# Optimization experiments

Hardware: AMD Instinct MI355X
Metric: run time of the kernel (lower is better)

## Reference

```python
import jax, jax.numpy as jnp
import numpy as np

B, N, CIN, H, OUT, L, K = 8, 512, 64, 64, 64, 256, 3
EPS = 1e-5


def setup_inputs() -> dict:
    key = jax.random.key(0)
    ks = jax.random.split(key, 12)
    def unif(k, shape, fan):
        s = 1.0 / np.sqrt(fan)
        return jax.random.uniform(k, shape, jnp.float32, -s, s)
    return {
        "x": jax.random.normal(ks[0], (B, N, CIN, L), jnp.float32),
        "adj": jax.random.uniform(ks[1], (B, N, N), jnp.float32),
        # temp_conv1: Conv1d(CIN->H, k=3)
        "w1": unif(ks[2], (H, CIN, K), CIN * K),
        "b1": unif(ks[3], (H,), CIN * K),
        # graph_conv: Linear-style (H,H) + bias, stdv=1/sqrt(out_features)
        "gw": unif(ks[4], (H, H), H),
        "gb": unif(ks[5], (H,), H),
        # temp_conv2: Conv1d(H->OUT, k=3)
        "w2": unif(ks[6], (OUT, H, K), H * K),
        "b2": unif(ks[7], (OUT,), H * K),
        # residual: Conv1d(CIN->OUT, k=1) == pointwise linear
        "wr": unif(ks[8], (OUT, CIN), CIN),
        "br": unif(ks[9], (OUT,), CIN),
        # BatchNorm2d(OUT) affine params
        "gamma": jnp.ones((OUT,), jnp.float32),
        "beta": jnp.zeros((OUT,), jnp.float32),
    }


def _conv1d(x, w, b, pad):
    # x: (B, N, C, L) -> flatten node dim into batch, NCH conv
    b_, n_, c, l = x.shape
    y = jax.lax.conv_general_dilated(
        x.reshape(b_ * n_, c, l), w, window_strides=(1,),
        padding=[(pad, pad)], dimension_numbers=("NCH", "OIH", "NCH"))
    y = y + b[None, :, None]
    return y.reshape(b_, n_, w.shape[0], l)


def reference(x, adj, w1, b1, gw, gb, w2, b2, wr, br, gamma, beta):
    pad = (K - 1) // 2
    # residual branch: 1x1 conv over channels
    residual = jnp.einsum("bncl,oc->bnol", x, wr) + br[None, None, :, None]
    # temporal conv 1
    out = _conv1d(x, w1, b1, pad)                      # (B,N,H,L)
    # graph conv over all timesteps at once (replaces per-t Python loop)
    xw = jnp.einsum("bnhl,hd->bndl", out, gw)          # (B,N,H,L)
    out = jnp.einsum("bnm,bmdl->bndl", adj, xw) + gb[None, None, :, None]
    # temporal conv 2
    out = _conv1d(out, w2, b2, pad)                    # (B,N,OUT,L)
    out = out + residual
    # BatchNorm2d over channel axis (training-mode batch stats, biased var)
    mean = jnp.mean(out, axis=(0, 1, 3), keepdims=True)
    var = jnp.mean(jnp.square(out - mean), axis=(0, 1, 3), keepdims=True)
    out = (out - mean) * jax.lax.rsqrt(var + EPS)
    out = out * gamma[None, None, :, None] + beta[None, None, :, None]
    return jax.nn.relu(out)
```

## Files before the change

kernel.cpp:

```cpp
#include <hip/hip_runtime.h>
#include <hip/hip_bf16.h>
#include <stdint.h>


typedef unsigned short u16;
typedef unsigned int   u32;
typedef __attribute__((ext_vector_type(8))) short           bf16x8;
typedef __attribute__((ext_vector_type(8))) unsigned short  u16x8;
typedef __attribute__((ext_vector_type(4))) unsigned short  u16x4;
typedef __attribute__((ext_vector_type(4))) float           f32x4;

__device__ __forceinline__ float bf2f(u16 v){
  union { u32 u; float f; } x; x.u = ((u32)v) << 16; return x.f;
}
__device__ __forceinline__ u16 f2bf(float f){
  __hip_bfloat16 h = __float2bfloat16(f);
  return *reinterpret_cast<u16*>(&h);
}
__device__ __forceinline__ u32 swz(int row, int cbyte){
  return (u32)(row * 128) + (u32)(cbyte ^ ((row & 7) << 4));
}

__global__ __launch_bounds__(256) void k_prep(const float* __restrict__ w1, const float* __restrict__ b1,
    const float* __restrict__ gw, const float* __restrict__ w2, const float* __restrict__ wr,
    u16* __restrict__ w1g, float* __restrict__ b1g, u16* __restrict__ w2t, u16* __restrict__ wrt){
  const int gt = blockIdx.x * 256 + threadIdx.x, gs = gridDim.x * 256;
  for (int e = gt; e < 12288; e += gs){
    int tap = e >> 12, rem = e & 4095, o = rem >> 6, c = rem & 63;
    w2t[e] = f2bf(w2[(o * 64 + c) * 3 + tap]);
    float s = 0.f;
    for (int h = 0; h < 64; ++h)
      s += gw[h * 64 + o] * w1[(h * 64 + c) * 3 + tap];
    w1g[e] = f2bf(s);
  }
  for (int e = gt; e < 4096; e += gs) wrt[e] = f2bf(wr[e]);
  for (int d = gt; d < 64; d += gs){
    float s = 0.f;
    for (int h = 0; h < 64; ++h) s += b1[h] * gw[h * 64 + d];
    b1g[d] = s;
  }
}

__global__ __launch_bounds__(256) void k_p1(const float* __restrict__ x,
    const u16* __restrict__ w1g, const float* __restrict__ b1g,
    const u16* __restrict__ wrt, u16* __restrict__ outA, u16* __restrict__ outR){
  __shared__ u16 tile[16384];
  const int t = threadIdx.x;
  const size_t bn = (size_t)blockIdx.x + (size_t)blockIdx.y * 512;
  const float* xb = x + bn * 16384;

  {
    const int c0 = (t >> 3) * 2;
    #pragma unroll
    for (int v = 0; v < 8; ++v){
      const int l0 = (t & 7) * 4 + v * 32;
      f32x4 a = *(const f32x4*)(xb + (size_t)c0 * 256 + l0);
      f32x4 b = *(const f32x4*)(xb + (size_t)(c0 + 1) * 256 + l0);
      #pragma unroll
      for (int e = 0; e < 4; ++e){
        u32 p = (u32)f2bf(a[e]) | ((u32)f2bf(b[e]) << 16);
        *(u32*)((char*)tile + swz(l0 + e, c0 * 2)) = p;
      }
    }
  }
  __syncthreads();
  const int w = t >> 6, ln = t & 63, lq = ln >> 4, lr = ln & 15;
  const bf16x8 z8 = {};

  {
    f32x4 racc[4][4];
    #pragma unroll
    for (int i = 0; i < 4; ++i)
      #pragma unroll
      for (int j = 0; j < 4; ++j) racc[i][j] = (f32x4){0.f, 0.f, 0.f, 0.f};
    #pragma unroll
    for (int kk = 0; kk < 2; ++kk){
      bf16x8 A[4];
      #pragma unroll
      for (int fo = 0; fo < 4; ++fo)
        A[fo] = *(const bf16x8*)(wrt + (fo * 16 + lr) * 64 + kk * 32 + lq * 8);
      #pragma unroll
      for (int fc = 0; fc < 4; ++fc){
        int l = w * 64 + fc * 16 + lr;
        bf16x8 B = *(const bf16x8*)((char*)tile + swz(l, kk * 64 + lq * 16));
        #pragma unroll
        for (int fo = 0; fo < 4; ++fo)
          racc[fo][fc] = __builtin_amdgcn_mfma_f32_16x16x32_bf16(A[fo], B, racc[fo][fc], 0, 0, 0);
      }
    }
    #pragma unroll
    for (int v = 0; v < 8; ++v){
      u16x8 ov;
      const int fo = v >> 1;
      #pragma unroll
      for (int h = 0; h < 2; ++h){
        const int fc = (v & 1) * 2 + h;
        #pragma unroll
        for (int r2 = 0; r2 < 4; ++r2)
          ov[h * 4 + r2] = f2bf(racc[fo][fc][r2]);
      }
      *(u16x8*)(outR + bn * 16384 + v * 2048 + t * 8) = ov;
    }
  }

  f32x4 acc[4][4];
  #pragma unroll
  for (int i = 0; i < 4; ++i)
    #pragma unroll
    for (int j = 0; j < 4; ++j) acc[i][j] = (f32x4){0.f, 0.f, 0.f, 0.f};
  #pragma unroll
  for (int tap = 0; tap < 3; ++tap){
    #pragma unroll
    for (int kk = 0; kk < 2; ++kk){
      bf16x8 A[4];
      #pragma unroll
      for (int fo = 0; fo < 4; ++fo)
        A[fo] = *(const bf16x8*)(w1g + tap * 4096 + (fo * 16 + lr) * 64 + kk * 32 + lq * 8);
      #pragma unroll
      for (int fc = 0; fc < 4; ++fc){
        int r = w * 64 + fc * 16 + lr + tap - 1;
        int rc = r < 0 ? 0 : (r > 255 ? 255 : r);
        bf16x8 B = *(const bf16x8*)((char*)tile + swz(rc, kk * 64 + lq * 16));
        if (r != rc) B = z8;
        #pragma unroll
        for (int fo = 0; fo < 4; ++fo)
          acc[fo][fc] = __builtin_amdgcn_mfma_f32_16x16x32_bf16(A[fo], B, acc[fo][fc], 0, 0, 0);
      }
    }
  }
  __syncthreads();
  #pragma unroll
  for (int fo = 0; fo < 4; ++fo){
    float bb[4];
    #pragma unroll
    for (int r2 = 0; r2 < 4; ++r2) bb[r2] = b1g[fo * 16 + lq * 4 + r2];
    #pragma unroll
    for (int fc = 0; fc < 4; ++fc){
      int l = w * 64 + fc * 16 + lr;
      #pragma unroll
      for (int r2 = 0; r2 < 4; ++r2){
        int d = fo * 16 + lq * 4 + r2;
        *(u16*)((char*)tile + l * 128 + ((2 * d) ^ ((l & 7) << 4))) = f2bf(acc[fo][fc][r2] + bb[r2]);
      }
    }
  }
  __syncthreads();
  u16* op = outA + bn * 16384;
  #pragma unroll
  for (int v = 0; v < 8; ++v){
    int flat = v * 2048 + t * 8;
    int l = flat >> 6, d0 = flat & 63;
    u16x8 val = *(const u16x8*)((char*)tile + l * 128 + ((d0 * 2) ^ ((l & 7) << 4)));
    *(u16x8*)(op + flat) = val;
  }
}

__global__ __launch_bounds__(256) void k_p3(const u16* __restrict__ xw,
    const float* __restrict__ adj, const float* __restrict__ gbv, u16* __restrict__ outB){
  __shared__ u16 At[8192];
  __shared__ u16 Bt[8192];
  const int t = threadIdx.x;
  const int wg = ((blockIdx.x & 7) << 9) | ((int)blockIdx.x >> 3);
  const int jt = wg & 127, nt = (wg >> 7) & 3, b = wg >> 9;
  const float* adjb = adj + ((size_t)b * 512 + (size_t)nt * 128) * 512;
  const u16* Xb = xw + (size_t)b * 8388608 + (size_t)jt * 128;
  const int w = t >> 6, ln = t & 63, lq = ln >> 4, lr = ln & 15;
  const int wrow = w >> 1, wcol = w & 1;
  const int mpair = t & 31, jq = t >> 5;
  f32x4 acc[4][4];
  #pragma unroll
  for (int i = 0; i < 4; ++i)
    #pragma unroll
    for (int j = 0; j < 4; ++j) acc[i][j] = (f32x4){0.f, 0.f, 0.f, 0.f};

  f32x4 ra[8];
  u16x8 rb[4];
  auto LOADK = [&](int ks){
    #pragma unroll
    for (int it = 0; it < 8; ++it){
      int c = it * 256 + t;
      int row = c >> 4, mc = c & 15;
      ra[it] = *(const f32x4*)(adjb + (size_t)row * 512 + ks * 64 + mc * 4);
    }
    const u16* s0 = Xb + (size_t)(ks * 64 + mpair * 2) * 16384 + jq * 16;
    const u16* s1 = s0 + 16384;
    #pragma unroll
    for (int v2 = 0; v2 < 2; ++v2){
      rb[v2 * 2]     = *(const u16x8*)(s0 + v2 * 8);
      rb[v2 * 2 + 1] = *(const u16x8*)(s1 + v2 * 8);
    }
  };

  LOADK(0);
  for (int ks = 0; ks < 8; ++ks){
    #pragma unroll
    for (int it = 0; it < 8; ++it){
      int c = it * 256 + t;
      int row = c >> 4, mc = c & 15;
      u16x4 pk;
      #pragma unroll
      for (int e = 0; e < 4; ++e) pk[e] = f2bf(ra[it][e]);
      *(u16x4*)((char*)At + (u32)(row * 128) + (u32)((mc * 8) ^ ((row & 7) << 4))) = pk;
    }
    #pragma unroll
    for (int v2 = 0; v2 < 2; ++v2){
      #pragma unroll
      for (int e = 0; e < 8; ++e){
        u32 p = (u32)(u16)rb[v2 * 2][e] | ((u32)(u16)rb[v2 * 2 + 1][e] << 16);
        *(u32*)((char*)Bt + swz(jq * 16 + v2 * 8 + e, mpair * 4)) = p;
      }
    }
    __syncthreads();
    if (ks < 7) LOADK(ks + 1);
    #pragma unroll
    for (int kk = 0; kk < 2; ++kk){
      bf16x8 Af[4], Bf[4];
      #pragma unroll
      for (int f = 0; f < 4; ++f){
        int rA = wrow * 64 + f * 16 + lr;
        Af[f] = *(const bf16x8*)((char*)At + swz(rA, kk * 64 + lq * 16));
        int rB = wcol * 64 + f * 16 + lr;
        Bf[f] = *(const bf16x8*)((char*)Bt + swz(rB, kk * 64 + lq * 16));
      }
      #pragma unroll
      for (int fr = 0; fr < 4; ++fr)
        #pragma unroll
        for (int fc = 0; fc < 4; ++fc)
          acc[fr][fc] = __builtin_amdgcn_mfma_f32_16x16x32_bf16(Af[fr], Bf[fc], acc[fr][fc], 0, 0, 0);
    }
    __syncthreads();
  }
  float gbl[4];
  #pragma unroll
  for (int fc = 0; fc < 4; ++fc) gbl[fc] = gbv[fc * 16 + lr];
  u16* ob = outB + ((size_t)b * 512 + (size_t)nt * 128) * 16384 + (size_t)jt * 128;
  #pragma unroll
  for (int fr = 0; fr < 4; ++fr)
    #pragma unroll
    for (int fc = 0; fc < 4; ++fc)
      #pragma unroll
      for (int r2 = 0; r2 < 4; ++r2){
        int n_ = wrow * 64 + fr * 16 + lq * 4 + r2;
        int j_ = wcol * 64 + fc * 16 + lr;
        ob[(size_t)n_ * 16384 + j_] = f2bf(acc[fr][fc][r2] + gbl[fc]);
      }
}

__global__ __launch_bounds__(256) void k_p4(const u16* __restrict__ g,
    const u16* __restrict__ resv, const u16* __restrict__ w2t,
    const float* __restrict__ b2v, const float* __restrict__ brv,
    u16* __restrict__ outP, float* __restrict__ spart){
  __shared__ u16 gt2[16384];
  __shared__ float sc2[512];
  const int t = threadIdx.x;
  const size_t bn = (size_t)blockIdx.x + (size_t)blockIdx.y * 512;
  const u16* gb = g + bn * 16384;
  #pragma unroll
  for (int v = 0; v < 8; ++v){
    int flat = v * 2048 + t * 8;
    int l = flat >> 6, d0 = flat & 63;
    u16x8 val = *(const u16x8*)(gb + flat);
    *(u16x8*)((char*)gt2 + l * 128 + ((d0 * 2) ^ ((l & 7) << 4))) = val;
  }
  __syncthreads();
  const int w = t >> 6, ln = t & 63, lq = ln >> 4, lr = ln & 15;
  const bf16x8 z8 = {};

  u16x8 rv[8];
  #pragma unroll
  for (int v = 0; v < 8; ++v) rv[v] = *(const u16x8*)(resv + bn * 16384 + v * 2048 + t * 8);

  f32x4 acc[4][4];
  #pragma unroll
  for (int i = 0; i < 4; ++i)
    #pragma unroll
    for (int j = 0; j < 4; ++j) acc[i][j] = (f32x4){0.f, 0.f, 0.f, 0.f};

  #pragma unroll
  for (int tap = 0; tap < 3; ++tap){
    #pragma unroll
    for (int kk = 0; kk < 2; ++kk){
      bf16x8 A[4];
      #pragma unroll
      for (int fo = 0; fo < 4; ++fo)
        A[fo] = *(const bf16x8*)(w2t + tap * 4096 + (fo * 16 + lr) * 64 + kk * 32 + lq * 8);
      #pragma unroll
      for (int fc = 0; fc < 4; ++fc){
        int r = w * 64 + fc * 16 + lr + tap - 1;
        int rc = r < 0 ? 0 : (r > 255 ? 255 : r);
        bf16x8 B = *(const bf16x8*)((char*)gt2 + swz(rc, kk * 64 + lq * 16));
        if (r != rc) B = z8;
        #pragma unroll
        for (int fo = 0; fo < 4; ++fo)
          acc[fo][fc] = __builtin_amdgcn_mfma_f32_16x16x32_bf16(A[fo], B, acc[fo][fc], 0, 0, 0);
      }
    }
  }
  __syncthreads();

  float psum[16], psq[16];
  #pragma unroll
  for (int i = 0; i < 16; ++i){ psum[i] = 0.f; psq[i] = 0.f; }
  #pragma unroll
  for (int fo = 0; fo < 4; ++fo){
    float bb[4];
    #pragma unroll
    for (int r2 = 0; r2 < 4; ++r2){
      int o = fo * 16 + lq * 4 + r2;
      bb[r2] = b2v[o] + brv[o];
    }
    #pragma unroll
    for (int fc = 0; fc < 4; ++fc){
      int l = w * 64 + fc * 16 + lr;
      #pragma unroll
      for (int r2 = 0; r2 < 4; ++r2){
        float val = acc[fo][fc][r2] + bb[r2]
                  + bf2f(rv[fo * 2 + (fc >> 1)][(fc & 1) * 4 + r2]);
        int o = fo * 16 + lq * 4 + r2;
        gt2[o * 256 + (l ^ ((o & 7) * 8))] = f2bf(val);
        psum[fo * 4 + r2] += val;
        psq[fo * 4 + r2] += val * val;
      }
    }
  }
  #pragma unroll
  for (int i = 0; i < 16; ++i){
    #pragma unroll
    for (int m = 1; m < 16; m <<= 1){
      psum[i] += __shfl_xor(psum[i], m, 64);
      psq[i]  += __shfl_xor(psq[i],  m, 64);
    }
  }
  if (lr == 0){
    #pragma unroll
    for (int i = 0; i < 16; ++i){
      int o = (i >> 2) * 16 + lq * 4 + (i & 3);
      sc2[w * 128 + o]      = psum[i];
      sc2[w * 128 + 64 + o] = psq[i];
    }
  }
  __syncthreads();
  u16* op = outP + bn * 16384;
  #pragma unroll
  for (int v = 0; v < 8; ++v){
    int d = (t >> 5) + v * 8;
    int l0 = (t & 31) * 8;
    u16x8 val = *(const u16x8*)(gt2 + d * 256 + (l0 ^ ((d & 7) * 8)));
    *(u16x8*)(op + v * 2048 + t * 8) = val;
  }
  if (t < 128){
    float tot = sc2[t] + sc2[128 + t] + sc2[256 + t] + sc2[384 + t];
    spart[(size_t)t * 4096 + bn] = tot;
  }
}

__global__ __launch_bounds__(256) void k_p5(const float* __restrict__ part, float* __restrict__ fin){
  const int o = blockIdx.x, t = threadIdx.x;
  float s1 = 0.f, s2 = 0.f;
  for (int k = t; k < 4096; k += 256){
    s1 += part[(size_t)o * 4096 + k];
    s2 += part[(size_t)(64 + o) * 4096 + k];
  }
  #pragma unroll
  for (int m = 32; m; m >>= 1){
    s1 += __shfl_down(s1, m, 64);
    s2 += __shfl_down(s2, m, 64);
  }
  __shared__ float red[8];
  if ((t & 63) == 0){ red[(t >> 6) * 2] = s1; red[(t >> 6) * 2 + 1] = s2; }
  __syncthreads();
  if (t == 0){
    float S1 = red[0] + red[2] + red[4] + red[6];
    float S2 = red[1] + red[3] + red[5] + red[7];
    const float invN = 1.f / 1048576.f;
    float mean = S1 * invN;
    float var = S2 * invN - mean * mean;
    fin[o] = mean;
    fin[64 + o] = rsqrtf(var + 1e-5f);
  }
}

__global__ __launch_bounds__(256) void k_p6(const u16* __restrict__ pre, const float* __restrict__ fin,
    const float* __restrict__ gamma, const float* __restrict__ beta, float* __restrict__ out){
  __shared__ float ssca[64], soff[64];
  const int tt = threadIdx.x;
  if (tt < 64){
    float sc = fin[64 + tt] * gamma[tt];
    ssca[tt] = sc;
    soff[tt] = beta[tt] - fin[tt] * sc;
  }
  __syncthreads();
  const size_t nchunk = 8388608;
  for (size_t i = (size_t)blockIdx.x * 256 + tt; i < nchunk; i += (size_t)gridDim.x * 256){
    int o = (int)((i >> 5) & 63);
    float sca = ssca[o], off = soff[o];
    u16x8 v = *(const u16x8*)(pre + i * 8);
    f32x4 oa, ob;
    #pragma unroll
    for (int e = 0; e < 4; ++e){
      float f0 = bf2f(v[e]) * sca + off;
      float f1 = bf2f(v[4 + e]) * sca + off;
      oa[e] = f0 > 0.f ? f0 : 0.f;
      ob[e] = f1 > 0.f ? f1 : 0.f;
    }
    *(f32x4*)(out + i * 8)     = oa;
    *(f32x4*)(out + i * 8 + 4) = ob;
  }
}

extern "C" void kernel_launch(void* const* d_in, const int* in_sizes, int n_in,
                              void* d_out, int out_size, void* d_ws, size_t ws_size,
                              hipStream_t stream){
  const float* x     = (const float*)d_in[0];
  const float* adj   = (const float*)d_in[1];
  const float* w1    = (const float*)d_in[2];
  const float* b1    = (const float*)d_in[3];
  const float* gw    = (const float*)d_in[4];
  const float* gb    = (const float*)d_in[5];
  const float* w2    = (const float*)d_in[6];
  const float* b2    = (const float*)d_in[7];
  const float* wr    = (const float*)d_in[8];
  const float* br    = (const float*)d_in[9];
  const float* gamma = (const float*)d_in[10];
  const float* beta  = (const float*)d_in[11];
  (void)in_sizes; (void)n_in; (void)out_size; (void)ws_size;

  char* ws = (char*)d_ws;
  u16*   bufA  = (u16*)ws;
  float* spart = (float*)(ws + 134217728);
  float* sfin  = (float*)(ws + 136314880);
  u16*   w1g   = (u16*)(ws + 136315392);
  float* b1g   = (float*)(ws + 136339968);
  u16*   w2t   = (u16*)(ws + 136348160);
  u16*   wrt   = (u16*)(ws + 136372736);
  u16*   gbuf  = (u16*)d_out;
  u16*   bufR  = (u16*)d_out + 67108864;

  k_prep<<<16, 256, 0, stream>>>(w1, b1, gw, w2, wr, w1g, b1g, w2t, wrt);
  k_p1<<<dim3(512, 8, 1), 256, 0, stream>>>(x, w1g, b1g, wrt, bufA, bufR);
  k_p3<<<4096, 256, 0, stream>>>(bufA, adj, gb, gbuf);
  k_p4<<<dim3(512, 8, 1), 256, 0, stream>>>(gbuf, bufR, w2t, b2, br, bufA, spart);
  k_p5<<<64, 256, 0, stream>>>(spart, sfin);
  k_p6<<<2048, 256, 0, stream>>>(bufA, sfin, gamma, beta, (float*)d_out);
}
```

Measured before the change: 538.9 us.

## Make temporal-conv2 kernel loop over eight tiles with double-buffered async LDS prefetch

The second temporal-conv kernel now launches 512 blocks, and each block processes 8 consecutive (batch, node) tiles in a loop. The next tile's activations are prefetched into a second LDS buffer with global_load_lds while the current tile runs its MFMAs. BatchNorm partial sums are accumulated across the 8 tiles, so the partial buffer and the reduction kernel shrink from 4096 to 512 entries per channel. The cost is double the LDS per block and fewer blocks in flight. Correctness of the prefetch relies on hand-placed vmcnt, lgkmcnt and barrier waits.

```diff
diff --git a/kernel.cpp b/kernel.cpp
--- a/kernel.cpp
+++ b/kernel.cpp
@@ -250,79 +250,117 @@
     const u16* __restrict__ resv, const u16* __restrict__ w2t,
     const float* __restrict__ b2v, const float* __restrict__ brv,
     u16* __restrict__ outP, float* __restrict__ spart){
-  __shared__ u16 gt2[16384];
+  __shared__ u16 lbuf[32768];
   __shared__ float sc2[512];
   const int t = threadIdx.x;
-  const size_t bn = (size_t)blockIdx.x + (size_t)blockIdx.y * 512;
-  const u16* gb = g + bn * 16384;
-  #pragma unroll
-  for (int v = 0; v < 8; ++v){
-    int flat = v * 2048 + t * 8;
-    int l = flat >> 6, d0 = flat & 63;
-    u16x8 val = *(const u16x8*)(gb + flat);
-    *(u16x8*)((char*)gt2 + l * 128 + ((d0 * 2) ^ ((l & 7) << 4))) = val;
-  }
-  __syncthreads();
   const int w = t >> 6, ln = t & 63, lq = ln >> 4, lr = ln & 15;
+  const int blk = blockIdx.x;
   const bf16x8 z8 = {};
 
-  u16x8 rv[8];
-  #pragma unroll
-  for (int v = 0; v < 8; ++v) rv[v] = *(const u16x8*)(resv + bn * 16384 + v * 2048 + t * 8);
-
-  f32x4 acc[4][4];
-  #pragma unroll
-  for (int i = 0; i < 4; ++i)
-    #pragma unroll
-    for (int j = 0; j < 4; ++j) acc[i][j] = (f32x4){0.f, 0.f, 0.f, 0.f};
-
-  #pragma unroll
-  for (int tap = 0; tap < 3; ++tap){
-    #pragma unroll
-    for (int kk = 0; kk < 2; ++kk){
-      bf16x8 A[4];
-      #pragma unroll
-      for (int fo = 0; fo < 4; ++fo)
-        A[fo] = *(const bf16x8*)(w2t + tap * 4096 + (fo * 16 + lr) * 64 + kk * 32 + lq * 8);
-      #pragma unroll
-      for (int fc = 0; fc < 4; ++fc){
-        int r = w * 64 + fc * 16 + lr + tap - 1;
-        int rc = r < 0 ? 0 : (r > 255 ? 255 : r);
-        bf16x8 B = *(const bf16x8*)((char*)gt2 + swz(rc, kk * 64 + lq * 16));
-        if (r != rc) B = z8;
-        #pragma unroll
-        for (int fo = 0; fo < 4; ++fo)
-          acc[fo][fc] = __builtin_amdgcn_mfma_f32_16x16x32_bf16(A[fo], B, acc[fo][fc], 0, 0, 0);
-      }
-    }
-  }
-  __syncthreads();
-
-  float psum[16], psq[16];
-  #pragma unroll
-  for (int i = 0; i < 16; ++i){ psum[i] = 0.f; psq[i] = 0.f; }
-  #pragma unroll
-  for (int fo = 0; fo < 4; ++fo){
-    float bb[4];
+  auto DMA = [&](int tile, int buf){
+    const u16* gsrc = g + ((size_t)blk * 8 + tile) * 16384;
+    #pragma unroll
+    for (int i = 0; i < 8; ++i){
+      const int row = w * 64 + i * 8 + (ln >> 3);
+      const int c = ln & 7;
+      const u16* src = gsrc + (size_t)row * 64 + (size_t)((c ^ (row & 7)) * 8);
+      u16* dst = lbuf + buf * 16384 + w * 4096 + i * 512;
+      __builtin_amdgcn_global_load_lds(
+          (const __attribute__((address_space(1))) void*)src,
+          (__attribute__((address_space(3))) void*)dst, 16, 0, 0);
+    }
+  };
+
+  float bball[16];
+  #pragma unroll
+  for (int fo = 0; fo < 4; ++fo)
     #pragma unroll
     for (int r2 = 0; r2 < 4; ++r2){
       int o = fo * 16 + lq * 4 + r2;
-      bb[r2] = b2v[o] + brv[o];
-    }
-    #pragma unroll
-    for (int fc = 0; fc < 4; ++fc){
-      int l = w * 64 + fc * 16 + lr;
-      #pragma unroll
-      for (int r2 = 0; r2 < 4; ++r2){
-        float val = acc[fo][fc][r2] + bb[r2]
-                  + bf2f(rv[fo * 2 + (fc >> 1)][(fc & 1) * 4 + r2]);
-        int o = fo * 16 + lq * 4 + r2;
-        gt2[o * 256 + (l ^ ((o & 7) * 8))] = f2bf(val);
-        psum[fo * 4 + r2] += val;
-        psq[fo * 4 + r2] += val * val;
-      }
-    }
-  }
+      bball[fo * 4 + r2] = b2v[o] + brv[o];
+    }
+  float psum[16], psq[16];
+  #pragma unroll
+  for (int i = 0; i < 16; ++i){ psum[i] = 0.f; psq[i] = 0.f; }
+
+  DMA(0, 0);
+  for (int tt = 0; tt < 8; ++tt){
+    const size_t bn = (size_t)blk * 8 + tt;
+    u16* cur = lbuf + (tt & 1) * 16384;
+    if (tt == 0) asm volatile("s_waitcnt vmcnt(0)" ::: "memory");
+    else         asm volatile("s_waitcnt vmcnt(16)" ::: "memory");
+    __builtin_amdgcn_sched_barrier(0);
+    __builtin_amdgcn_s_barrier();
+    __builtin_amdgcn_sched_barrier(0);
+    if (tt < 7) DMA(tt + 1, (tt + 1) & 1);
+    __builtin_amdgcn_sched_barrier(0);
+
+    u16x8 rv[8];
+    #pragma unroll
+    for (int v = 0; v < 8; ++v) rv[v] = *(const u16x8*)(resv + bn * 16384 + v * 2048 + t * 8);
+
+    f32x4 acc[4][4];
+    #pragma unroll
+    for (int i = 0; i < 4; ++i)
+      #pragma unroll
+      for (int j = 0; j < 4; ++j) acc[i][j] = (f32x4){0.f, 0.f, 0.f, 0.f};
+    #pragma unroll
+    for (int tap = 0; tap < 3; ++tap){
+      #pragma unroll
+      for (int kk = 0; kk < 2; ++kk){
+        bf16x8 A[4];
+        #pragma unroll
+        for (int fo = 0; fo < 4; ++fo)
+          A[fo] = *(const bf16x8*)(w2t + tap * 4096 + (fo * 16 + lr) * 64 + kk * 32 + lq * 8);
+        #pragma unroll
+        for (int fc = 0; fc < 4; ++fc){
+          int r = w * 64 + fc * 16 + lr + tap - 1;
+          int rc = r < 0 ? 0 : (r > 255 ? 255 : r);
+          bf16x8 B = *(const bf16x8*)((char*)cur + swz(rc, kk * 64 + lq * 16));
+          if (r != rc) B = z8;
+          #pragma unroll
+          for (int fo = 0; fo < 4; ++fo)
+            acc[fo][fc] = __builtin_amdgcn_mfma_f32_16x16x32_bf16(A[fo], B, acc[fo][fc], 0, 0, 0);
+        }
+      }
+    }
+    __builtin_amdgcn_sched_barrier(0);
+    asm volatile("s_waitcnt lgkmcnt(0)" ::: "memory");
+    __builtin_amdgcn_sched_barrier(0);
+    __builtin_amdgcn_s_barrier();
+    __builtin_amdgcn_sched_barrier(0);
+    #pragma unroll
+    for (int fo = 0; fo < 4; ++fo){
+      #pragma unroll
+      for (int fc = 0; fc < 4; ++fc){
+        int l = w * 64 + fc * 16 + lr;
+        #pragma unroll
+        for (int r2 = 0; r2 < 4; ++r2){
+          float val = acc[fo][fc][r2] + bball[fo * 4 + r2]
+                    + bf2f(rv[fo * 2 + (fc >> 1)][(fc & 1) * 4 + r2]);
+          int o = fo * 16 + lq * 4 + r2;
+          cur[o * 256 + (l ^ ((o & 7) * 8))] = f2bf(val);
+          psum[fo * 4 + r2] += val;
+          psq[fo * 4 + r2] += val * val;
+        }
+      }
+    }
+    __builtin_amdgcn_sched_barrier(0);
+    asm volatile("s_waitcnt lgkmcnt(0)" ::: "memory");
+    __builtin_amdgcn_sched_barrier(0);
+    __builtin_amdgcn_s_barrier();
+    __builtin_amdgcn_sched_barrier(0);
+    u16* op = outP + bn * 16384;
+    #pragma unroll
+    for (int v = 0; v < 8; ++v){
+      int d = (t >> 5) + v * 8;
+      int l0 = (t & 31) * 8;
+      u16x8 val = *(const u16x8*)(cur + d * 256 + (l0 ^ ((d & 7) * 8)));
+      *(u16x8*)(op + v * 2048 + t * 8) = val;
+    }
+    __builtin_amdgcn_sched_barrier(0);
+  }
+
   #pragma unroll
   for (int i = 0; i < 16; ++i){
     #pragma unroll
@@ -340,26 +378,18 @@
     }
   }
   __syncthreads();
-  u16* op = outP + bn * 16384;
-  #pragma unroll
-  for (int v = 0; v < 8; ++v){
-    int d = (t >> 5) + v * 8;
-    int l0 = (t & 31) * 8;
-    u16x8 val = *(const u16x8*)(gt2 + d * 256 + (l0 ^ ((d & 7) * 8)));
-    *(u16x8*)(op + v * 2048 + t * 8) = val;
-  }
   if (t < 128){
     float tot = sc2[t] + sc2[128 + t] + sc2[256 + t] + sc2[384 + t];
-    spart[(size_t)t * 4096 + bn] = tot;
+    spart[(size_t)t * 512 + blk] = tot;
   }
 }
 
 __global__ __launch_bounds__(256) void k_p5(const float* __restrict__ part, float* __restrict__ fin){
   const int o = blockIdx.x, t = threadIdx.x;
   float s1 = 0.f, s2 = 0.f;
-  for (int k = t; k < 4096; k += 256){
-    s1 += part[(size_t)o * 4096 + k];
-    s2 += part[(size_t)(64 + o) * 4096 + k];
+  for (int k = t; k < 512; k += 256){
+    s1 += part[(size_t)o * 512 + k];
+    s2 += part[(size_t)(64 + o) * 512 + k];
   }
   #pragma unroll
   for (int m = 32; m; m >>= 1){
@@ -439,7 +469,7 @@
   k_prep<<<16, 256, 0, stream>>>(w1, b1, gw, w2, wr, w1g, b1g, w2t, wrt);
   k_p1<<<dim3(512, 8, 1), 256, 0, stream>>>(x, w1g, b1g, wrt, bufA, bufR);
   k_p3<<<4096, 256, 0, stream>>>(bufA, adj, gb, gbuf);
-  k_p4<<<dim3(512, 8, 1), 256, 0, stream>>>(gbuf, bufR, w2t, b2, br, bufA, spart);
+  k_p4<<<512, 256, 0, stream>>>(gbuf, bufR, w2t, b2, br, bufA, spart);
   k_p5<<<64, 256, 0, stream>>>(spart, sfin);
   k_p6<<<2048, 256, 0, stream>>>(bufA, sfin, gamma, beta, (float*)d_out);
 }
```

After: 541.3 us. About the same (+0.4%).

## Apply second temporal conv before adjacency matmul to fuse it into first kernel

Applied to the files above, without the earlier changes.

Because the adjacency product is linear over nodes and the second conv acts per node over time and channel, the conv is applied first, inside k_p1, while the tile is still in shared memory. The graph bias is folded into a per-timestep bias that handles the zero-padded boundary timesteps at l=0 and l=255. k_p4 becomes a plain residual add plus BatchNorm statistics pass, which removes a full read and transpose pass with MFMA. The cost is extra register and MFMA work in k_p1, plus one more bf16 rounding before the adjacency matmul.

```diff
diff --git a/kernel.cpp b/kernel.cpp
--- a/kernel.cpp
+++ b/kernel.cpp
@@ -23,7 +23,9 @@
 
 __global__ __launch_bounds__(256) void k_prep(const float* __restrict__ w1, const float* __restrict__ b1,
     const float* __restrict__ gw, const float* __restrict__ w2, const float* __restrict__ wr,
-    u16* __restrict__ w1g, float* __restrict__ b1g, u16* __restrict__ w2t, u16* __restrict__ wrt){
+    const float* __restrict__ gb, const float* __restrict__ b2, const float* __restrict__ br,
+    u16* __restrict__ w1g, float* __restrict__ b1g, u16* __restrict__ w2t, u16* __restrict__ wrt,
+    float* __restrict__ bias3){
   const int gt = blockIdx.x * 256 + threadIdx.x, gs = gridDim.x * 256;
   for (int e = gt; e < 12288; e += gs){
     int tap = e >> 12, rem = e & 4095, o = rem >> 6, c = rem & 63;
@@ -39,11 +41,25 @@
     for (int h = 0; h < 64; ++h) s += b1[h] * gw[h * 64 + d];
     b1g[d] = s;
   }
+  for (int o = gt; o < 64; o += gs){
+    float s0 = 0.f, s1 = 0.f, s2 = 0.f;
+    for (int d = 0; d < 64; ++d){
+      float g_ = gb[d];
+      s0 += w2[(o * 64 + d) * 3 + 0] * g_;
+      s1 += w2[(o * 64 + d) * 3 + 1] * g_;
+      s2 += w2[(o * 64 + d) * 3 + 2] * g_;
+    }
+    float bb = b2[o] + br[o];
+    bias3[o]       = bb + s1 + s2;
+    bias3[64 + o]  = bb + s0 + s1 + s2;
+    bias3[128 + o] = bb + s0 + s1;
+  }
 }
 
 __global__ __launch_bounds__(256) void k_p1(const float* __restrict__ x,
     const u16* __restrict__ w1g, const float* __restrict__ b1g,
-    const u16* __restrict__ wrt, u16* __restrict__ outA, u16* __restrict__ outR){
+    const u16* __restrict__ wrt, const u16* __restrict__ w2t,
+    u16* __restrict__ outA, u16* __restrict__ outR){
   __shared__ u16 tile[16384];
   const int t = threadIdx.x;
   const size_t bn = (size_t)blockIdx.x + (size_t)blockIdx.y * 512;
@@ -145,6 +161,45 @@
     }
   }
   __syncthreads();
+
+  f32x4 acc2[4][4];
+  #pragma unroll
+  for (int i = 0; i < 4; ++i)
+    #pragma unroll
+    for (int j = 0; j < 4; ++j) acc2[i][j] = (f32x4){0.f, 0.f, 0.f, 0.f};
+  #pragma unroll
+  for (int tap = 0; tap < 3; ++tap){
+    #pragma unroll
+    for (int kk = 0; kk < 2; ++kk){
+      bf16x8 A[4];
+      #pragma unroll
+      for (int fo = 0; fo < 4; ++fo)
+        A[fo] = *(const bf16x8*)(w2t + tap * 4096 + (fo * 16 + lr) * 64 + kk * 32 + lq * 8);
+      #pragma unroll
+      for (int fc = 0; fc < 4; ++fc){
+        int r = w * 64 + fc * 16 + lr + tap - 1;
+        int rc = r < 0 ? 0 : (r > 255 ? 255 : r);
+        bf16x8 B = *(const bf16x8*)((char*)tile + swz(rc, kk * 64 + lq * 16));
+        if (r != rc) B = z8;
+        #pragma unroll
+        for (int fo = 0; fo < 4; ++fo)
+          acc2[fo][fc] = __builtin_amdgcn_mfma_f32_16x16x32_bf16(A[fo], B, acc2[fo][fc], 0, 0, 0);
+      }
+    }
+  }
+  __syncthreads();
+  #pragma unroll
+  for (int fo = 0; fo < 4; ++fo)
+    #pragma unroll
+    for (int fc = 0; fc < 4; ++fc){
+      int l = w * 64 + fc * 16 + lr;
+      #pragma unroll
+      for (int r2 = 0; r2 < 4; ++r2){
+        int d = fo * 16 + lq * 4 + r2;
+        *(u16*)((char*)tile + l * 128 + ((2 * d) ^ ((l & 7) << 4))) = f2bf(acc2[fo][fc][r2]);
+      }
+    }
+  __syncthreads();
   u16* op = outA + bn * 16384;
   #pragma unroll
   for (int v = 0; v < 8; ++v){
@@ -155,15 +210,15 @@
   }
 }
 
-__global__ __launch_bounds__(256) void k_p3(const u16* __restrict__ xw,
-    const float* __restrict__ adj, const float* __restrict__ gbv, u16* __restrict__ outB){
+__global__ __launch_bounds__(256) void k_p3(const u16* __restrict__ y,
+    const float* __restrict__ adj, const float* __restrict__ bias3, u16* __restrict__ outB){
   __shared__ u16 At[8192];
   __shared__ u16 Bt[8192];
   const int t = threadIdx.x;
   const int wg = ((blockIdx.x & 7) << 9) | ((int)blockIdx.x >> 3);
   const int jt = wg & 127, nt = (wg >> 7) & 3, b = wg >> 9;
   const float* adjb = adj + ((size_t)b * 512 + (size_t)nt * 128) * 512;
-  const u16* Xb = xw + (size_t)b * 8388608 + (size_t)jt * 128;
+  const u16* Xb = y + (size_t)b * 8388608 + (size_t)jt * 128;
   const int w = t >> 6, ln = t & 63, lq = ln >> 4, lr = ln & 15;
   const int wrow = w >> 1, wcol = w & 1;
   const int mpair = t & 31, jq = t >> 5;
@@ -230,9 +285,11 @@
     }
     __syncthreads();
   }
+  const int l = jt * 2 + wcol;
+  const float* bt = bias3 + ((l == 0) ? 0 : (l == 255 ? 128 : 64));
   float gbl[4];
   #pragma unroll
-  for (int fc = 0; fc < 4; ++fc) gbl[fc] = gbv[fc * 16 + lr];
+  for (int fc = 0; fc < 4; ++fc) gbl[fc] = bt[fc * 16 + lr];
   u16* ob = outB + ((size_t)b * 512 + (size_t)nt * 128) * 16384 + (size_t)jt * 128;
   #pragma unroll
   for (int fr = 0; fr < 4; ++fr)
@@ -246,112 +303,92 @@
       }
 }
 
-__global__ __launch_bounds__(256) void k_p4(const u16* __restrict__ g,
-    const u16* __restrict__ resv, const u16* __restrict__ w2t,
-    const float* __restrict__ b2v, const float* __restrict__ brv,
-    u16* __restrict__ outP, float* __restrict__ spart){
-  __shared__ u16 gt2[16384];
-  __shared__ float sc2[512];
+__global__ __launch_bounds__(256) void k_p4(const u16* __restrict__ core,
+    const u16* __restrict__ resv, u16* __restrict__ outP, float* __restrict__ spart){
+  __shared__ u16 plane[16384];
+  __shared__ float sc2[128];
   const int t = threadIdx.x;
-  const size_t bn = (size_t)blockIdx.x + (size_t)blockIdx.y * 512;
-  const u16* gb = g + bn * 16384;
-  #pragma unroll
-  for (int v = 0; v < 8; ++v){
-    int flat = v * 2048 + t * 8;
-    int l = flat >> 6, d0 = flat & 63;
-    u16x8 val = *(const u16x8*)(gb + flat);
-    *(u16x8*)((char*)gt2 + l * 128 + ((d0 * 2) ^ ((l & 7) << 4))) = val;
-  }
-  __syncthreads();
-  const int w = t >> 6, ln = t & 63, lq = ln >> 4, lr = ln & 15;
-  const bf16x8 z8 = {};
-
-  u16x8 rv[8];
-  #pragma unroll
-  for (int v = 0; v < 8; ++v) rv[v] = *(const u16x8*)(resv + bn * 16384 + v * 2048 + t * 8);
-
-  f32x4 acc[4][4];
-  #pragma unroll
-  for (int i = 0; i < 4; ++i)
-    #pragma unroll
-    for (int j = 0; j < 4; ++j) acc[i][j] = (f32x4){0.f, 0.f, 0.f, 0.f};
-
-  #pragma unroll
-  for (int tap = 0; tap < 3; ++tap){
-    #pragma unroll
-    for (int kk = 0; kk < 2; ++kk){
-      bf16x8 A[4];
-      #pragma unroll
-      for (int fo = 0; fo < 4; ++fo)
-        A[fo] = *(const bf16x8*)(w2t + tap * 4096 + (fo * 16 + lr) * 64 + kk * 32 + lq * 8);
-      #pragma unroll
-      for (int fc = 0; fc < 4; ++fc){
-        int r = w * 64 + fc * 16 + lr + tap - 1;
-        int rc = r < 0 ? 0 : (r > 255 ? 255 : r);
-        bf16x8 B = *(const bf16x8*)((char*)gt2 + swz(rc, kk * 64 + lq * 16));
-        if (r != rc) B = z8;
-        #pragma unroll
-        for (int fo = 0; fo < 4; ++fo)
-          acc[fo][fc] = __builtin_amdgcn_mfma_f32_16x16x32_bf16(A[fo], B, acc[fo][fc], 0, 0, 0);
-      }
-    }
-  }
-  __syncthreads();
-
-  float psum[16], psq[16];
-  #pragma unroll
-  for (int i = 0; i < 16; ++i){ psum[i] = 0.f; psq[i] = 0.f; }
-  #pragma unroll
-  for (int fo = 0; fo < 4; ++fo){
-    float bb[4];
-    #pragma unroll
-    for (int r2 = 0; r2 < 4; ++r2){
-      int o = fo * 16 + lq * 4 + r2;
-      bb[r2] = b2v[o] + brv[o];
-    }
-    #pragma unroll
-    for (int fc = 0; fc < 4; ++fc){
-      int l = w * 64 + fc * 16 + lr;
+  const size_t bn = (size_t)blockIdx.x;
+  const int w = t >> 6, lq = (t >> 4) & 3, lr = t & 15;
+
+  u16x8 cv[8], rv[8];
+  #pragma unroll
+  for (int v = 0; v < 8; ++v){
+    cv[v] = *(const u16x8*)(core + bn * 16384 + v * 2048 + t * 8);
+    rv[v] = *(const u16x8*)(resv + bn * 16384 + v * 2048 + t * 8);
+  }
+  #pragma unroll
+  for (int v = 0; v < 8; ++v){
+    const int l = v * 32 + (t >> 3);
+    const int d0 = (t & 7) * 8;
+    #pragma unroll
+    for (int e = 0; e < 8; ++e){
+      const int o = d0 + e;
+      plane[o * 256 + (l ^ ((o & 7) * 8))] = (u16)cv[v][e];
+    }
+  }
+  __syncthreads();
+  u16x8 c8[8];
+  #pragma unroll
+  for (int v = 0; v < 8; ++v){
+    const int d = (t >> 5) + v * 8;
+    const int l0 = (t & 31) * 8;
+    c8[v] = *(const u16x8*)(plane + d * 256 + (l0 ^ ((d & 7) * 8)));
+  }
+  __syncthreads();
+  #pragma unroll
+  for (int v = 0; v < 8; ++v){
+    const int fo = v >> 1;
+    #pragma unroll
+    for (int h = 0; h < 2; ++h){
+      const int fc = (v & 1) * 2 + h;
+      const int l = w * 64 + fc * 16 + lr;
       #pragma unroll
       for (int r2 = 0; r2 < 4; ++r2){
-        float val = acc[fo][fc][r2] + bb[r2]
-                  + bf2f(rv[fo * 2 + (fc >> 1)][(fc & 1) * 4 + r2]);
-        int o = fo * 16 + lq * 4 + r2;
-        gt2[o * 256 + (l ^ ((o & 7) * 8))] = f2bf(val);
-        psum[fo * 4 + r2] += val;
-        psq[fo * 4 + r2] += val * val;
-      }
-    }
-  }
-  #pragma unroll
-  for (int i = 0; i < 16; ++i){
-    #pragma unroll
-    for (int m = 1; m < 16; m <<= 1){
-      psum[i] += __shfl_xor(psum[i], m, 64);
-      psq[i]  += __shfl_xor(psq[i],  m, 64);
-    }
-  }
-  if (lr == 0){
-    #pragma unroll
-    for (int i = 0; i < 16; ++i){
-      int o = (i >> 2) * 16 + lq * 4 + (i & 3);
-      sc2[w * 128 + o]      = psum[i];
-      sc2[w * 128 + 64 + o] = psq[i];
-    }
-  }
-  __syncthreads();
+        const int o = fo * 16 + lq * 4 + r2;
+        plane[o * 256 + (l ^ ((o & 7) * 8))] = (u16)rv[v][h * 4 + r2];
+      }
+    }
+  }
+  __syncthreads();
+  float psum[8], psq[8];
+  #pragma unroll
+  for (int i = 0; i < 8; ++i){ psum[i] = 0.f; psq[i] = 0.f; }
   u16* op = outP + bn * 16384;
   #pragma unroll
   for (int v = 0; v < 8; ++v){
-    int d = (t >> 5) + v * 8;
-    int l0 = (t & 31) * 8;
-    u16x8 val = *(const u16x8*)(gt2 + d * 256 + (l0 ^ ((d & 7) * 8)));
-    *(u16x8*)(op + v * 2048 + t * 8) = val;
-  }
-  if (t < 128){
-    float tot = sc2[t] + sc2[128 + t] + sc2[256 + t] + sc2[384 + t];
-    spart[(size_t)t * 4096 + bn] = tot;
-  }
+    const int d = (t >> 5) + v * 8;
+    const int l0 = (t & 31) * 8;
+    u16x8 r8 = *(const u16x8*)(plane + d * 256 + (l0 ^ ((d & 7) * 8)));
+    u16x8 ov;
+    #pragma unroll
+    for (int e = 0; e < 8; ++e){
+      float val = bf2f((u16)c8[v][e]) + bf2f((u16)r8[e]);
+      ov[e] = f2bf(val);
+      psum[v] += val;
+      psq[v]  += val * val;
+    }
+    *(u16x8*)(op + v * 2048 + t * 8) = ov;
+  }
+  #pragma unroll
+  for (int v = 0; v < 8; ++v){
+    #pragma unroll
+    for (int m = 1; m < 32; m <<= 1){
+      psum[v] += __shfl_xor(psum[v], m, 64);
+      psq[v]  += __shfl_xor(psq[v],  m, 64);
+    }
+  }
+  if ((t & 31) == 0){
+    const int g = t >> 5;
+    #pragma unroll
+    for (int v = 0; v < 8; ++v){
+      const int o = g + v * 8;
+      sc2[o]      = psum[v];
+      sc2[64 + o] = psq[v];
+    }
+  }
+  __syncthreads();
+  if (t < 128) spart[(size_t)t * 4096 + bn] = sc2[t];
 }
 
 __global__ __launch_bounds__(256) void k_p5(const float* __restrict__ part, float* __restrict__ fin){
@@ -433,13 +470,14 @@
   float* b1g   = (float*)(ws + 136339968);
   u16*   w2t   = (u16*)(ws + 136348160);
   u16*   wrt   = (u16*)(ws + 136372736);
+  float* bias3 = (float*)(ws + 136380928);
   u16*   gbuf  = (u16*)d_out;
   u16*   bufR  = (u16*)d_out + 67108864;
 
-  k_prep<<<16, 256, 0, stream>>>(w1, b1, gw, w2, wr, w1g, b1g, w2t, wrt);
-  k_p1<<<dim3(512, 8, 1), 256, 0, stream>>>(x, w1g, b1g, wrt, bufA, bufR);
-  k_p3<<<4096, 256, 0, stream>>>(bufA, adj, gb, gbuf);
-  k_p4<<<dim3(512, 8, 1), 256, 0, stream>>>(gbuf, bufR, w2t, b2, br, bufA, spart);
+  k_prep<<<16, 256, 0, stream>>>(w1, b1, gw, w2, wr, gb, b2, br, w1g, b1g, w2t, wrt, bias3);
+  k_p1<<<dim3(512, 8, 1), 256, 0, stream>>>(x, w1g, b1g, wrt, w2t, bufA, bufR);
+  k_p3<<<4096, 256, 0, stream>>>(bufA, adj, bias3, gbuf);
+  k_p4<<<4096, 256, 0, stream>>>(gbuf, bufR, bufA, spart);
   k_p5<<<64, 256, 0, stream>>>(spart, sfin);
   k_p6<<<2048, 256, 0, stream>>>(bufA, sfin, gamma, beta, (float*)d_out);
 }
```

New measurement: 556.2 us. +3.2%, slower.
